# Kernel tuning notes

Hardware: AMD Instinct MI355X
Metric: run time of the kernel (lower is better)

Reference implementation:

```python
import jax, jax.numpy as jnp
import numpy as np

N_ATOMS = 500000
N_BONDS = 1000000
MAX_NB = 6
ATOM_FDIM = 133
BOND_FDIM = 14
HIDDEN = 128
MP_DEPTH = 3
ATOMS_PER_MOL = 20


def setup_inputs() -> dict:
    key = jax.random.key(0)
    ks = jax.random.split(key, 12)
    inp = {
        "f_atoms": jax.random.normal(ks[0], (N_ATOMS, ATOM_FDIM), jnp.float32),
        "f_bonds": jax.random.normal(ks[1], (N_BONDS, BOND_FDIM), jnp.float32),
        "Wi_w": jax.random.normal(ks[2], (HIDDEN, ATOM_FDIM), jnp.float32) * 0.05,
        "Wi_b": jax.random.normal(ks[3], (HIDDEN,), jnp.float32) * 0.05,
        "Wh_w": jax.random.normal(ks[4], (HIDDEN, HIDDEN + BOND_FDIM), jnp.float32) * 0.05,
        "Wh_b": jax.random.normal(ks[5], (HIDDEN,), jnp.float32) * 0.05,
        "Wo_w": jax.random.normal(ks[6], (HIDDEN, ATOM_FDIM + HIDDEN), jnp.float32) * 0.05,
        "Wo_b": jax.random.normal(ks[7], (HIDDEN,), jnp.float32) * 0.05,
        "ffn_w": jax.random.normal(ks[8], (1, HIDDEN), jnp.float32) * 0.05,
        "ffn_b": jax.random.normal(ks[9], (1,), jnp.float32) * 0.05,
        "a2a": jax.random.randint(ks[10], (N_ATOMS, MAX_NB), 0, N_ATOMS, jnp.int32),
        "a2b": jax.random.randint(ks[11], (N_ATOMS, MAX_NB), 0, N_BONDS, jnp.int32),
        "atoms_per_mol": ATOMS_PER_MOL,
    }
    return inp


def reference(f_atoms, f_bonds, Wi_w, Wi_b, Wh_w, Wh_b, Wo_w, Wo_b, ffn_w, ffn_b,
              a2a, a2b, atoms_per_mol):
    # W_i + ReLU: initial atom messages
    x = f_atoms @ Wi_w.T + Wi_b                     # [N_atoms, H]
    message = jax.nn.relu(x)
    # pre-aggregate bond features once (constant across depths)
    nei_f_bonds_sum = f_bonds[a2b].sum(axis=1)      # [N_atoms, BOND_FDIM]
    for _ in range(MP_DEPTH - 1):
        # gather neighbor messages and sum (index_select_ND + sum(dim=1));
        # concat(msg_gather, bond_gather).sum(1) == concat(sum(msg), sum(bond))
        nei_a_message = message[a2a].sum(axis=1)    # [N_atoms, H]
        nei = jnp.concatenate([nei_a_message, nei_f_bonds_sum], axis=1)
        message = jax.nn.relu(x + nei @ Wh_w.T + Wh_b)
        # dropout is identity in eval mode
    # final aggregation + W_o
    a_message = message[a2a].sum(axis=1)            # [N_atoms, H]
    a_input = jnp.concatenate([f_atoms, a_message], axis=1)
    atom_hiddens = jax.nn.relu(a_input @ Wo_w.T + Wo_b)
    # max readout per molecule (equal-size a_scope of atoms_per_mol)
    n_atoms, h = atom_hiddens.shape
    mol_vecs = atom_hiddens.reshape(n_atoms // atoms_per_mol, atoms_per_mol, h).max(axis=1)
    # FFN head (NN_depth=1): Dropout (identity) + Linear(H -> 1)
    return mol_vecs @ ffn_w.T + ffn_b               # [n_mols, 1]
```

## Files before the change

### kernel.cpp

```cpp
#include <hip/hip_runtime.h>
#include <hip/hip_bf16.h>

#define N_ATOMS   500000
#define N_BONDS   1000000
#define MAX_NB    6
#define ATOM_FDIM 133
#define BOND_FDIM 14
#define HIDDEN    128
#define N_MOLS    25000
#define APM       20

typedef __attribute__((ext_vector_type(8))) short short8;
typedef __attribute__((ext_vector_type(4))) float f32x4;
typedef unsigned short u16;
typedef unsigned int   u32;

__device__ __forceinline__ float bf2f(u16 u) {
    u32 t = ((u32)u) << 16;
    return __builtin_bit_cast(float, t);
}
__device__ __forceinline__ u16 f2bf(float f) {
    u32 t = __builtin_bit_cast(u32, f);
    t += 0x7FFFu + ((t >> 16) & 1u);
    return (u16)(t >> 16);
}

__device__ __forceinline__ void gl16(const u16* g, u16* l) {
    __builtin_amdgcn_global_load_lds(
        (__attribute__((address_space(1))) void*)(g),
        (__attribute__((address_space(3))) void*)(l), 16, 0, 0);
}

__global__ void prep_weights(const float* __restrict__ Wi, const float* __restrict__ Wh,
                             const float* __restrict__ Wo,
                             u16* __restrict__ Wip, u16* __restrict__ Whp, u16* __restrict__ Wop) {
    int stride = gridDim.x * blockDim.x;
    int tid = blockIdx.x * blockDim.x + threadIdx.x;
    for (int i = tid; i < 128 * 160; i += stride) {
        int r = i / 160, c = i % 160;
        Wip[i] = (c < 133) ? f2bf(Wi[r * 133 + c]) : (u16)0;
        Whp[i] = (c < 142) ? f2bf(Wh[r * 142 + c]) : (u16)0;
    }
    for (int i = tid; i < 128 * 288; i += stride) {
        int r = i / 288, c = i % 288;
        float v = 0.f;
        if (c < 133)      v = Wo[r * 261 + c];
        else if (c >= 160) v = Wo[r * 261 + (c - 27)];
        Wop[i] = f2bf(v);
    }
}

#define CROWS 24
__global__ __launch_bounds__(256) void fa_convert(const float* __restrict__ fa, u16* __restrict__ out) {
    __shared__ float buf[CROWS * 133];
    const long row0 = (long)blockIdx.x * CROWS;
    const int rows = (int)((N_ATOMS - row0) < CROWS ? (N_ATOMS - row0) : CROWS);
    const float* src = fa + row0 * ATOM_FDIM;
    if (rows == CROWS) {
        for (int i = threadIdx.x; i < (CROWS * 133) / 4; i += 256)
            *(float4*)(&buf[i * 4]) = *(const float4*)(src + i * 4);
    } else {
        for (int i = threadIdx.x; i < rows * 133; i += 256) buf[i] = src[i];
    }
    __syncthreads();
    for (int j = threadIdx.x; j < rows * 20; j += 256) {
        int r = j / 20, c8 = (j % 20) * 8;
        u16 u[8];
#pragma unroll
        for (int e = 0; e < 8; e++) {
            int c = c8 + e;
            u[e] = (c < ATOM_FDIM) ? f2bf(buf[r * 133 + c]) : (u16)0;
        }
        uint4 v;
        v.x = (u32)u[0] | ((u32)u[1] << 16);
        v.y = (u32)u[2] | ((u32)u[3] << 16);
        v.z = (u32)u[4] | ((u32)u[5] << 16);
        v.w = (u32)u[6] | ((u32)u[7] << 16);
        *(uint4*)(out + (row0 + r) * 160 + c8) = v;
    }
}

__global__ __launch_bounds__(256) void bond_gather(const float* __restrict__ fb, const int* __restrict__ a2b,
                                                   u16* __restrict__ outp) {
    long t = (long)blockIdx.x * 256 + threadIdx.x;
    int atom = (int)(t >> 4);
    int c2   = (int)(t & 15);
    if (atom >= N_ATOMS) return;
    int c0 = 2 * c2, c1 = c0 + 1;
    float s0 = 0.f, s1 = 0.f;
    if (c0 < BOND_FDIM) {
#pragma unroll
        for (int j = 0; j < MAX_NB; j++) {
            int idx = a2b[atom * 6 + j];
            const float* row = fb + (long)idx * BOND_FDIM;
            s0 += row[c0];
            if (c1 < BOND_FDIM) s1 += row[c1];
        }
    }
    *(u32*)(outp + (long)atom * 32 + c0) = (u32)f2bf(s0) | ((u32)f2bf(s1) << 16);
}

__global__ __launch_bounds__(256) void gather_relu_sum(const u16* __restrict__ src,
                                                       const int* __restrict__ a2a,
                                                       u16* __restrict__ dst) {
    long t = (long)blockIdx.x * 256 + threadIdx.x;
    int atom = (int)(t >> 4);
    int c8   = (int)(t & 15) << 3;
    float s[8] = {0, 0, 0, 0, 0, 0, 0, 0};
#pragma unroll
    for (int j = 0; j < MAX_NB; j++) {
        int idx = a2a[atom * 6 + j];
        uint4 v = *(const uint4*)(src + (long)idx * 128 + c8);
        u32 w[4] = {v.x, v.y, v.z, v.w};
#pragma unroll
        for (int q = 0; q < 4; q++) {
            s[2 * q]     += fmaxf(__builtin_bit_cast(float, w[q] << 16), 0.f);
            s[2 * q + 1] += fmaxf(__builtin_bit_cast(float, w[q] & 0xFFFF0000u), 0.f);
        }
    }
    uint4 o;
    o.x = (u32)f2bf(s[0]) | ((u32)f2bf(s[1]) << 16);
    o.y = (u32)f2bf(s[2]) | ((u32)f2bf(s[3]) << 16);
    o.z = (u32)f2bf(s[4]) | ((u32)f2bf(s[5]) << 16);
    o.w = (u32)f2bf(s[6]) | ((u32)f2bf(s[7]) << 16);
    *(uint4*)(dst + (long)atom * 128 + c8) = o;
}

#define ISSUE_SLOT(d, t)                                                              \
    do {                                                                              \
        if ((t) < NT) {                                                               \
            long r_ = (t) * TILE + wave * 16 + lrow;                                  \
            if (r_ > N_ATOMS - 1) r_ = N_ATOMS - 1;                                   \
            if constexpr (KB0 > 0) {                                                  \
                const u16* p_ = A0 + r_ * (long)ldA0 + kg * 8;                        \
                _Pragma("unroll") for (int kb = 0; kb < KB0; kb++)                    \
                    a[d][kb] = *(const uint4*)(p_ + kb * 32);                         \
            }                                                                         \
            if constexpr (KB1 > 0) {                                                  \
                const u16* p_ = A1 + r_ * (long)ldA1 + kg * 8;                        \
                _Pragma("unroll") for (int kb = 0; kb < KB1; kb++)                    \
                    a[d][KB0 + kb] = *(const uint4*)(p_ + kb * 32);                   \
            }                                                                         \
            if constexpr (ADDX) {                                                     \
                _Pragma("unroll") for (int n = 0; n < 8; n++)                         \
                    xv[d][n] = *(const uint2*)(Xadd + r_ * 128 + n * 16 + kg * 4);    \
            }                                                                         \
        }                                                                             \
    } while (0)

template <int KB0, int KB1, bool ADDX, bool BIAS, int DEPTH>
__global__ __launch_bounds__(512, 2) void gemm_rp(
    const u16* __restrict__ A0, int ldA0,
    const u16* __restrict__ A1, int ldA1,
    const u16* __restrict__ Wp, const float* __restrict__ bias,
    const u16* __restrict__ Xadd, u16* __restrict__ Out) {
    constexpr int KB    = KB0 + KB1;
    constexpr int KP    = KB * 32;
    constexpr int TILE  = 128;
    constexpr long NT   = (N_ATOMS + TILE - 1) / TILE;
    constexpr int WSLOTS = KB * 8;
    constexpr int NWAIT = (DEPTH - 1) * (KB + 8 + (ADDX ? 8 : 0));
    static_assert(NWAIT <= 63, "vmcnt range");
    __shared__ __align__(16) u16 WL[WSLOTS * 512];

    const int lane = threadIdx.x & 63;
    const int wave = threadIdx.x >> 6;
    const int lrow = lane & 15;
    const int kg   = lane >> 4;

    for (int s = wave; s < WSLOTS; s += 8) {
        int kb = s >> 3, n = s & 7;
        gl16(Wp + (n * 16 + lrow) * KP + kb * 32 + kg * 8, WL + s * 512);
    }
    asm volatile("s_waitcnt vmcnt(0)" ::: "memory");
    __syncthreads();

    float4 b4[8];
#pragma unroll
    for (int n = 0; n < 8; n++)
        b4[n] = BIAS ? *(const float4*)(bias + n * 16 + kg * 4) : (float4){0.f, 0.f, 0.f, 0.f};

    const int G  = gridDim.x;
    const long t0 = blockIdx.x;

    uint4 a[DEPTH][KB];
    uint2 xv[DEPTH][ADDX ? 8 : 1];

#pragma unroll
    for (int d = 0; d < DEPTH; d++) {
        long tp = t0 + (long)d * G;
        ISSUE_SLOT(d, tp);
    }
    __builtin_amdgcn_sched_barrier(0);

#pragma unroll 1
    for (long tt = t0; tt < NT; tt += (long)DEPTH * G) {
#pragma unroll
        for (int d = 0; d < DEPTH; d++) {
            long t = tt + (long)d * G;
            if (t < NT) {
                asm volatile("s_waitcnt vmcnt(%0)" :: "n"(NWAIT) : "memory");
                __builtin_amdgcn_sched_barrier(0);

                f32x4 acc[8];
#pragma unroll
                for (int n = 0; n < 8; n++) acc[n] = (f32x4){0.f, 0.f, 0.f, 0.f};
#pragma unroll
                for (int kb = 0; kb < KB; kb++) {
                    short8 af = __builtin_bit_cast(short8, a[d][kb]);
#pragma unroll
                    for (int n = 0; n < 8; n++) {
                        short8 bf = *(const short8*)(WL + (kb * 8 + n) * 512 + lane * 8);
                        acc[n] = __builtin_amdgcn_mfma_f32_16x16x32_bf16(bf, af, acc[n], 0, 0, 0);
                    }
                }

                long r = t * TILE + wave * 16 + lrow;
                if (r < N_ATOMS) {
#pragma unroll
                    for (int n = 0; n < 8; n++) {
                        float v0 = acc[n][0] + b4[n].x;
                        float v1 = acc[n][1] + b4[n].y;
                        float v2 = acc[n][2] + b4[n].z;
                        float v3 = acc[n][3] + b4[n].w;
                        if constexpr (ADDX) {
                            v0 += __builtin_bit_cast(float, xv[d][n].x << 16);
                            v1 += __builtin_bit_cast(float, xv[d][n].x & 0xFFFF0000u);
                            v2 += __builtin_bit_cast(float, xv[d][n].y << 16);
                            v3 += __builtin_bit_cast(float, xv[d][n].y & 0xFFFF0000u);
                        }
                        uint2 o;
                        o.x = (u32)f2bf(v0) | ((u32)f2bf(v1) << 16);
                        o.y = (u32)f2bf(v2) | ((u32)f2bf(v3) << 16);
                        *(uint2*)(Out + r * 128 + n * 16 + kg * 4) = o;
                    }
                }
                __builtin_amdgcn_sched_barrier(0);
                long tf = t + (long)DEPTH * G;
                ISSUE_SLOT(d, tf);
                __builtin_amdgcn_sched_barrier(0);
            }
        }
    }
}

__global__ __launch_bounds__(256) void readout(const u16* __restrict__ ah,
                                               const float* __restrict__ ffn_w,
                                               const float* __restrict__ ffn_b,
                                               float* __restrict__ out) {
    int mol  = blockIdx.x * 4 + (threadIdx.x >> 6);
    int lane = threadIdx.x & 63;
    if (mol >= N_MOLS) return;
    float m0 = -1e30f, m1 = -1e30f;
    const u16* base = ah + (long)mol * APM * 128 + 2 * lane;
#pragma unroll
    for (int a = 0; a < APM; a++) {
        u32 v = *(const u32*)(base + a * 128);
        m0 = fmaxf(m0, bf2f((u16)(v & 0xFFFFu)));
        m1 = fmaxf(m1, bf2f((u16)(v >> 16)));
    }
    m0 = fmaxf(m0, 0.f);
    m1 = fmaxf(m1, 0.f);
    float p = m0 * ffn_w[2 * lane] + m1 * ffn_w[2 * lane + 1];
#pragma unroll
    for (int off = 32; off > 0; off >>= 1) p += __shfl_down(p, off);
    if (lane == 0) out[mol] = p + ffn_b[0];
}

extern "C" void kernel_launch(void* const* d_in, const int* in_sizes, int n_in,
                              void* d_out, int out_size, void* d_ws, size_t ws_size,
                              hipStream_t stream) {
    const float* f_atoms = (const float*)d_in[0];
    const float* f_bonds = (const float*)d_in[1];
    const float* Wi_w = (const float*)d_in[2];
    const float* Wi_b = (const float*)d_in[3];
    const float* Wh_w = (const float*)d_in[4];
    const float* Wh_b = (const float*)d_in[5];
    const float* Wo_w = (const float*)d_in[6];
    const float* Wo_b = (const float*)d_in[7];
    const float* ffn_w = (const float*)d_in[8];
    const float* ffn_b = (const float*)d_in[9];
    const int* a2a = (const int*)d_in[10];
    const int* a2b = (const int*)d_in[11];
    float* out = (float*)d_out;

    char* ws = (char*)d_ws;
    u16* fa    = (u16*)(ws);
    u16* xb    = (u16*)(ws + 160000000L);
    u16* msgA  = (u16*)(ws + 288000000L);
    u16* msgB  = (u16*)(ws + 416000000L);
    u16* nsum  = (u16*)(ws + 544000000L);
    u16* nbond = (u16*)(ws + 672000000L);
    u16* Wip   = (u16*)(ws + 704000000L);
    u16* Whp   = (u16*)(ws + 704040960L);
    u16* Wop   = (u16*)(ws + 704081920L);

    prep_weights<<<64, 256, 0, stream>>>(Wi_w, Wh_w, Wo_w, Wip, Whp, Wop);
    fa_convert<<<(N_ATOMS + CROWS - 1) / CROWS, 256, 0, stream>>>(f_atoms, fa);
    bond_gather<<<31250, 256, 0, stream>>>(f_bonds, a2b, nbond);

    gemm_rp<5, 0, false, true, 3><<<256, 512, 0, stream>>>(
        fa, 160, (const u16*)nullptr, 0, Wip, Wi_b, (const u16*)nullptr, xb);

    gather_relu_sum<<<31250, 256, 0, stream>>>(xb, a2a, nsum);
    gemm_rp<4, 1, true, true, 3><<<256, 512, 0, stream>>>(
        nsum, 128, nbond, 32, Whp, Wh_b, xb, msgA);
    gather_relu_sum<<<31250, 256, 0, stream>>>(msgA, a2a, nsum);
    gemm_rp<4, 1, true, true, 3><<<256, 512, 0, stream>>>(
        nsum, 128, nbond, 32, Whp, Wh_b, xb, msgB);
    gather_relu_sum<<<31250, 256, 0, stream>>>(msgB, a2a, nsum);
    gemm_rp<5, 4, false, true, 3><<<256, 512, 0, stream>>>(
        fa, 160, nsum, 128, Wop, Wo_b, (const u16*)nullptr, msgA);

    readout<<<6250, 256, 0, stream>>>(msgA, ffn_w, ffn_b, out);
}
```

Measured before the change: 897.7 us.

## Fuse fp32-to-bf16 atom conversion into the Wi GEMM and deepen Wh prefetch

Removes the separate fa_convert kernel. A new gemm_wi kernel loads f_atoms as fp32, converts it to bf16 fragments in registers, runs the Wi MFMA GEMM, and writes the padded bf16 atom features for the later Wo GEMM. This drops one full round-trip over the atom feature matrix and one launch, at the cost of unaligned fp32 row loads and more registers. Separately, the Wh GEMMs raise their prefetch depth from 3 to 4. The slot-issue guard is removed, so out-of-range tiles now clamp to the last row and always issue loads, which keeps the vmcnt accounting uniform.

New measurement: 873.8 us. -2.7%, faster.

```diff
diff --git a/kernel.cpp b/kernel.cpp
--- a/kernel.cpp
+++ b/kernel.cpp
@@ -23,6 +23,9 @@
     u32 t = __builtin_bit_cast(u32, f);
     t += 0x7FFFu + ((t >> 16) & 1u);
     return (u16)(t >> 16);
+}
+__device__ __forceinline__ u32 pk2(float a, float b) {
+    return (u32)f2bf(a) | ((u32)f2bf(b) << 16);
 }
 
 __device__ __forceinline__ void gl16(const u16* g, u16* l) {
@@ -50,36 +53,6 @@
     }
 }
 
-#define CROWS 24
-__global__ __launch_bounds__(256) void fa_convert(const float* __restrict__ fa, u16* __restrict__ out) {
-    __shared__ float buf[CROWS * 133];
-    const long row0 = (long)blockIdx.x * CROWS;
-    const int rows = (int)((N_ATOMS - row0) < CROWS ? (N_ATOMS - row0) : CROWS);
-    const float* src = fa + row0 * ATOM_FDIM;
-    if (rows == CROWS) {
-        for (int i = threadIdx.x; i < (CROWS * 133) / 4; i += 256)
-            *(float4*)(&buf[i * 4]) = *(const float4*)(src + i * 4);
-    } else {
-        for (int i = threadIdx.x; i < rows * 133; i += 256) buf[i] = src[i];
-    }
-    __syncthreads();
-    for (int j = threadIdx.x; j < rows * 20; j += 256) {
-        int r = j / 20, c8 = (j % 20) * 8;
-        u16 u[8];
-#pragma unroll
-        for (int e = 0; e < 8; e++) {
-            int c = c8 + e;
-            u[e] = (c < ATOM_FDIM) ? f2bf(buf[r * 133 + c]) : (u16)0;
-        }
-        uint4 v;
-        v.x = (u32)u[0] | ((u32)u[1] << 16);
-        v.y = (u32)u[2] | ((u32)u[3] << 16);
-        v.z = (u32)u[4] | ((u32)u[5] << 16);
-        v.w = (u32)u[6] | ((u32)u[7] << 16);
-        *(uint4*)(out + (row0 + r) * 160 + c8) = v;
-    }
-}
-
 __global__ __launch_bounds__(256) void bond_gather(const float* __restrict__ fb, const int* __restrict__ a2b,
                                                    u16* __restrict__ outp) {
     long t = (long)blockIdx.x * 256 + threadIdx.x;
@@ -97,7 +70,7 @@
             if (c1 < BOND_FDIM) s1 += row[c1];
         }
     }
-    *(u32*)(outp + (long)atom * 32 + c0) = (u32)f2bf(s0) | ((u32)f2bf(s1) << 16);
+    *(u32*)(outp + (long)atom * 32 + c0) = pk2(s0, s1);
 }
 
 __global__ __launch_bounds__(256) void gather_relu_sum(const u16* __restrict__ src,
@@ -119,32 +92,30 @@
         }
     }
     uint4 o;
-    o.x = (u32)f2bf(s[0]) | ((u32)f2bf(s[1]) << 16);
-    o.y = (u32)f2bf(s[2]) | ((u32)f2bf(s[3]) << 16);
-    o.z = (u32)f2bf(s[4]) | ((u32)f2bf(s[5]) << 16);
-    o.w = (u32)f2bf(s[6]) | ((u32)f2bf(s[7]) << 16);
+    o.x = pk2(s[0], s[1]);
+    o.y = pk2(s[2], s[3]);
+    o.z = pk2(s[4], s[5]);
+    o.w = pk2(s[6], s[7]);
     *(uint4*)(dst + (long)atom * 128 + c8) = o;
 }
 
 #define ISSUE_SLOT(d, t)                                                              \
     do {                                                                              \
-        if ((t) < NT) {                                                               \
-            long r_ = (t) * TILE + wave * 16 + lrow;                                  \
-            if (r_ > N_ATOMS - 1) r_ = N_ATOMS - 1;                                   \
-            if constexpr (KB0 > 0) {                                                  \
-                const u16* p_ = A0 + r_ * (long)ldA0 + kg * 8;                        \
-                _Pragma("unroll") for (int kb = 0; kb < KB0; kb++)                    \
-                    a[d][kb] = *(const uint4*)(p_ + kb * 32);                         \
-            }                                                                         \
-            if constexpr (KB1 > 0) {                                                  \
-                const u16* p_ = A1 + r_ * (long)ldA1 + kg * 8;                        \
-                _Pragma("unroll") for (int kb = 0; kb < KB1; kb++)                    \
-                    a[d][KB0 + kb] = *(const uint4*)(p_ + kb * 32);                   \
-            }                                                                         \
-            if constexpr (ADDX) {                                                     \
-                _Pragma("unroll") for (int n = 0; n < 8; n++)                         \
-                    xv[d][n] = *(const uint2*)(Xadd + r_ * 128 + n * 16 + kg * 4);    \
-            }                                                                         \
+        long r_ = (t) * TILE + wave * 16 + lrow;                                      \
+        if (r_ > N_ATOMS - 1) r_ = N_ATOMS - 1;                                       \
+        if constexpr (KB0 > 0) {                                                      \
+            const u16* p_ = A0 + r_ * (long)ldA0 + kg * 8;                            \
+            _Pragma("unroll") for (int kb = 0; kb < KB0; kb++)                        \
+                a[d][kb] = *(const uint4*)(p_ + kb * 32);                             \
+        }                                                                             \
+        if constexpr (KB1 > 0) {                                                      \
+            const u16* p_ = A1 + r_ * (long)ldA1 + kg * 8;                            \
+            _Pragma("unroll") for (int kb = 0; kb < KB1; kb++)                        \
+                a[d][KB0 + kb] = *(const uint4*)(p_ + kb * 32);                       \
+        }                                                                             \
+        if constexpr (ADDX) {                                                         \
+            _Pragma("unroll") for (int n = 0; n < 8; n++)                             \
+                xv[d][n] = *(const uint2*)(Xadd + r_ * 128 + n * 16 + kg * 4);        \
         }                                                                             \
     } while (0)
 
@@ -187,10 +158,7 @@
     uint2 xv[DEPTH][ADDX ? 8 : 1];
 
 #pragma unroll
-    for (int d = 0; d < DEPTH; d++) {
-        long tp = t0 + (long)d * G;
-        ISSUE_SLOT(d, tp);
-    }
+    for (int d = 0; d < DEPTH; d++) ISSUE_SLOT(d, t0 + (long)d * G);
     __builtin_amdgcn_sched_barrier(0);
 
 #pragma unroll 1
@@ -230,18 +198,146 @@
                             v3 += __builtin_bit_cast(float, xv[d][n].y & 0xFFFF0000u);
                         }
                         uint2 o;
-                        o.x = (u32)f2bf(v0) | ((u32)f2bf(v1) << 16);
-                        o.y = (u32)f2bf(v2) | ((u32)f2bf(v3) << 16);
+                        o.x = pk2(v0, v1);
+                        o.y = pk2(v2, v3);
                         *(uint2*)(Out + r * 128 + n * 16 + kg * 4) = o;
                     }
                 }
                 __builtin_amdgcn_sched_barrier(0);
-                long tf = t + (long)DEPTH * G;
-                ISSUE_SLOT(d, tf);
+                ISSUE_SLOT(d, t + (long)DEPTH * G);
                 __builtin_amdgcn_sched_barrier(0);
             }
         }
     }
+}
+
+__global__ __launch_bounds__(512, 2) void gemm_wi(
+    const float* __restrict__ FA, const u16* __restrict__ Wp,
+    const float* __restrict__ bias, u16* __restrict__ fa16, u16* __restrict__ Out) {
+    constexpr int KB = 5, KP = 160, TILE = 128;
+    constexpr long NT = (N_ATOMS + TILE - 1) / TILE;
+    constexpr int WSLOTS = KB * 8;
+    constexpr int DEPTH = 2;
+    constexpr int NWAIT = 23;
+    __shared__ __align__(16) u16 WL[WSLOTS * 512];
+
+    const int lane = threadIdx.x & 63;
+    const int wave = threadIdx.x >> 6;
+    const int lrow = lane & 15;
+    const int kg   = lane >> 4;
+
+    for (int s = wave; s < WSLOTS; s += 8) {
+        int kb = s >> 3, n = s & 7;
+        gl16(Wp + (n * 16 + lrow) * KP + kb * 32 + kg * 8, WL + s * 512);
+    }
+    asm volatile("s_waitcnt vmcnt(0)" ::: "memory");
+    __syncthreads();
+
+    float4 b4[8];
+#pragma unroll
+    for (int n = 0; n < 8; n++) b4[n] = *(const float4*)(bias + n * 16 + kg * 4);
+
+    const int G  = gridDim.x;
+    const long t0 = blockIdx.x;
+
+    uint4 af32[DEPTH][4][2];
+    uint4 a4[DEPTH];
+    float a4s[DEPTH];
+
+#define WI_ISSUE(d, t)                                                         \
+    do {                                                                       \
+        long r_ = (t) * TILE + wave * 16 + lrow;                               \
+        if (r_ > N_ATOMS - 1) r_ = N_ATOMS - 1;                                \
+        const float* p_ = FA + r_ * (long)ATOM_FDIM + kg * 8;                  \
+        _Pragma("unroll") for (int kb = 0; kb < 4; kb++) {                     \
+            af32[d][kb][0] = *(const uint4*)(p_ + kb * 32);                    \
+            af32[d][kb][1] = *(const uint4*)(p_ + kb * 32 + 4);                \
+        }                                                                      \
+        if (kg == 0) {                                                         \
+            const float* q_ = FA + r_ * (long)ATOM_FDIM + 128;                 \
+            a4[d]  = *(const uint4*)(q_);                                      \
+            a4s[d] = q_[4];                                                    \
+        }                                                                      \
+    } while (0)
+
+#pragma unroll
+    for (int d = 0; d < DEPTH; d++) WI_ISSUE(d, t0 + (long)d * G);
+    __builtin_amdgcn_sched_barrier(0);
+
+#pragma unroll 1
+    for (long tt = t0; tt < NT; tt += (long)DEPTH * G) {
+#pragma unroll
+        for (int d = 0; d < DEPTH; d++) {
+            long t = tt + (long)d * G;
+            if (t < NT) {
+                asm volatile("s_waitcnt vmcnt(%0)" :: "n"(NWAIT) : "memory");
+                __builtin_amdgcn_sched_barrier(0);
+
+                long r = t * TILE + wave * 16 + lrow;
+                bool wr = (r < N_ATOMS);
+
+                short8 frag[5];
+#pragma unroll
+                for (int kb = 0; kb < 4; kb++) {
+                    float f[8];
+                    f[0] = __builtin_bit_cast(float4, af32[d][kb][0]).x;
+                    f[1] = __builtin_bit_cast(float4, af32[d][kb][0]).y;
+                    f[2] = __builtin_bit_cast(float4, af32[d][kb][0]).z;
+                    f[3] = __builtin_bit_cast(float4, af32[d][kb][0]).w;
+                    f[4] = __builtin_bit_cast(float4, af32[d][kb][1]).x;
+                    f[5] = __builtin_bit_cast(float4, af32[d][kb][1]).y;
+                    f[6] = __builtin_bit_cast(float4, af32[d][kb][1]).z;
+                    f[7] = __builtin_bit_cast(float4, af32[d][kb][1]).w;
+                    uint4 pk;
+                    pk.x = pk2(f[0], f[1]);
+                    pk.y = pk2(f[2], f[3]);
+                    pk.z = pk2(f[4], f[5]);
+                    pk.w = pk2(f[6], f[7]);
+                    frag[kb] = __builtin_bit_cast(short8, pk);
+                }
+                {
+                    uint4 pk = (uint4){0, 0, 0, 0};
+                    if (kg == 0) {
+                        float4 q = __builtin_bit_cast(float4, a4[d]);
+                        pk.x = pk2(q.x, q.y);
+                        pk.y = pk2(q.z, q.w);
+                        pk.z = pk2(a4s[d], 0.f);
+                        pk.w = 0;
+                    }
+                    frag[4] = __builtin_bit_cast(short8, pk);
+                }
+
+                f32x4 acc[8];
+#pragma unroll
+                for (int n = 0; n < 8; n++) acc[n] = (f32x4){0.f, 0.f, 0.f, 0.f};
+#pragma unroll
+                for (int kb = 0; kb < 5; kb++) {
+#pragma unroll
+                    for (int n = 0; n < 8; n++) {
+                        short8 bf = *(const short8*)(WL + (kb * 8 + n) * 512 + lane * 8);
+                        acc[n] = __builtin_amdgcn_mfma_f32_16x16x32_bf16(bf, frag[kb], acc[n], 0, 0, 0);
+                    }
+                }
+
+                if (wr) {
+#pragma unroll
+                    for (int kb = 0; kb < 5; kb++)
+                        *(uint4*)(fa16 + r * 160 + kb * 32 + kg * 8) = __builtin_bit_cast(uint4, frag[kb]);
+#pragma unroll
+                    for (int n = 0; n < 8; n++) {
+                        uint2 o;
+                        o.x = pk2(acc[n][0] + b4[n].x, acc[n][1] + b4[n].y);
+                        o.y = pk2(acc[n][2] + b4[n].z, acc[n][3] + b4[n].w);
+                        *(uint2*)(Out + r * 128 + n * 16 + kg * 4) = o;
+                    }
+                }
+                __builtin_amdgcn_sched_barrier(0);
+                WI_ISSUE(d, t + (long)DEPTH * G);
+                __builtin_amdgcn_sched_barrier(0);
+            }
+        }
+    }
+#undef WI_ISSUE
 }
 
 __global__ __launch_bounds__(256) void readout(const u16* __restrict__ ah,
@@ -296,17 +392,15 @@
     u16* Wop   = (u16*)(ws + 704081920L);
 
     prep_weights<<<64, 256, 0, stream>>>(Wi_w, Wh_w, Wo_w, Wip, Whp, Wop);
-    fa_convert<<<(N_ATOMS + CROWS - 1) / CROWS, 256, 0, stream>>>(f_atoms, fa);
     bond_gather<<<31250, 256, 0, stream>>>(f_bonds, a2b, nbond);
 
-    gemm_rp<5, 0, false, true, 3><<<256, 512, 0, stream>>>(
-        fa, 160, (const u16*)nullptr, 0, Wip, Wi_b, (const u16*)nullptr, xb);
+    gemm_wi<<<256, 512, 0, stream>>>(f_atoms, Wip, Wi_b, fa, xb);
 
     gather_relu_sum<<<31250, 256, 0, stream>>>(xb, a2a, nsum);
-    gemm_rp<4, 1, true, true, 3><<<256, 512, 0, stream>>>(
+    gemm_rp<4, 1, true, true, 4><<<256, 512, 0, stream>>>(
         nsum, 128, nbond, 32, Whp, Wh_b, xb, msgA);
     gather_relu_sum<<<31250, 256, 0, stream>>>(msgA, a2a, nsum);
-    gemm_rp<4, 1, true, true, 3><<<256, 512, 0, stream>>>(
+    gemm_rp<4, 1, true, true, 4><<<256, 512, 0, stream>>>(
         nsum, 128, nbond, 32, Whp, Wh_b, xb, msgB);
     gather_relu_sum<<<31250, 256, 0, stream>>>(msgB, a2a, nsum);
     gemm_rp<5, 4, false, true, 3><<<256, 512, 0, stream>>>(
```
